# Performance work log

Hardware: AMD Instinct MI355X
Metric: run time of the kernel (lower is better)

The kernel has to match this reference:

```python
import jax, jax.numpy as jnp
import numpy as np

B, T, E, H, NT, NC = 256, 512, 200, 100, 100000, 5


def setup_inputs() -> dict:
    key = jax.random.key(0)
    ks = jax.random.split(key, 16)
    w = lambda i, shape: jax.random.normal(ks[i], shape, dtype=jnp.float32) * 0.05
    return {
        "txt": jax.random.randint(ks[0], (B, T), 0, NT),
        "lens": jax.random.randint(ks[1], (B,), 1, T + 1),
        "emb": w(2, (NT, E)),
        "W_ih": w(3, (3 * H, E)), "W_hh": w(4, (3 * H, H)),
        "b_ih": w(5, (3 * H,)), "b_hh": w(6, (3 * H,)),
        "W_lgr": w(7, (1, 2 * H)), "b_lgr": w(8, (1,)),
        "W_ts": w(9, (H, H)), "b_ts": w(10, (H,)),
        "W_ti": w(11, (H, H)), "b_ti": w(12, (H,)),
        "W_out": w(13, (NC, H)), "b_out": w(14, (NC,)),
    }


def reference(txt, lens, emb, W_ih, W_hh, b_ih, b_hh, W_lgr, b_lgr,
              W_ts, b_ts, W_ti, b_ti, W_out, b_out):
    bsz = txt.shape[0]
    # Embedding lookup with max_norm=1 renorm (torch nn.Embedding max_norm semantics)
    rows = emb[txt]  # (B,T,E)
    n = jnp.linalg.norm(rows, axis=-1, keepdims=True)
    emb_w = rows * jnp.where(n > 1.0, 1.0 / (n + 1e-7), 1.0)
    # eval mode: dropout is identity

    # ---- single-layer GRU (batch_first), gates in torch order r,z,n ----
    xp = emb_w @ W_ih.T + b_ih  # (B,T,3H), input projections precomputed

    def gru_step(h, x):
        hp = h @ W_hh.T + b_hh
        xr, xz, xn = jnp.split(x, 3, axis=-1)
        hr, hz, hn = jnp.split(hp, 3, axis=-1)
        r = jax.nn.sigmoid(xr + hr)
        z = jax.nn.sigmoid(xz + hz)
        ng = jnp.tanh(xn + r * hn)
        h = (1.0 - z) * ng + z * h
        return h, h

    h0 = jnp.zeros((bsz, H), jnp.float32)
    _, hs = jax.lax.scan(gru_step, h0, jnp.swapaxes(xp, 0, 1))
    rnn_out = jnp.swapaxes(hs, 0, 1)  # (B,T,H)

    # ---- cosine attention against an all-ones query ----
    inn = rnn_out / jnp.maximum(jnp.linalg.norm(rnn_out, axis=-1, keepdims=True), 1e-12)
    q = jnp.ones((bsz, H), jnp.float32)
    qn = q / jnp.maximum(jnp.linalg.norm(q, axis=-1, keepdims=True), 1e-12)
    att = jnp.einsum('bth,bh->bt', inn, qn) / H
    mask = (jnp.arange(T)[None, :] < lens[:, None]).astype(att.dtype)
    a_w = att * mask  # (B,T)

    # ---- gated-state recurrence ----
    z_all = jax.nn.relu(a_w)[..., None]          # (B,T,1)
    ti = rnn_out @ W_ti.T + b_ti                  # (B,T,H) trans_inp precomputed
    lgr_in = rnn_out @ W_lgr[:, :H].T             # (B,T,1) input half of lgr
    Wls = W_lgr[:, H:]                            # state half of lgr

    def rec_step(state, xs):
        ti_t, li_t, z_t = xs
        gate = jax.nn.sigmoid(li_t + state @ Wls.T + b_lgr)
        ns = jnp.tanh(ti_t + (gate * state) @ W_ts.T + b_ts)
        state = (1.0 - z_t) * state + z_t * ns
        return state, None

    xs = (jnp.swapaxes(ti, 0, 1), jnp.swapaxes(lgr_in, 0, 1), jnp.swapaxes(z_all, 0, 1))
    state, _ = jax.lax.scan(rec_step, jnp.zeros((bsz, H), jnp.float32), xs)
    return state @ W_out.T + b_out  # (B,NC)
```

## Files before the change

### kernel.cpp

```cpp
#include <hip/hip_runtime.h>

#define B_   256
#define T_   512
#define E_   200
#define H_   100
#define H3_  300
#define NC_  5

__device__ __forceinline__ void fma4(float4& acc, float a, const float4& w) {
    acc.x = fmaf(a, w.x, acc.x);
    acc.y = fmaf(a, w.y, acc.y);
    acc.z = fmaf(a, w.z, acc.z);
    acc.w = fmaf(a, w.w, acc.w);
}

#define KEEP4(v) asm volatile("" : "+v"((v).x), "+v"((v).y), "+v"((v).z), "+v"((v).w))

__device__ __forceinline__ void ldsbar() {
    asm volatile("s_waitcnt lgkmcnt(0)" ::: "memory");
    __builtin_amdgcn_s_barrier();
    __builtin_amdgcn_sched_barrier(0);
}

__global__ void k_pack(const float* __restrict__ W_ih, const float* __restrict__ W_ti,
                       const float* __restrict__ W_lgr,
                       float* __restrict__ wT, float* __restrict__ wcat) {
    int idx = blockIdx.x * 256 + threadIdx.x;
    if (idx < E_ * H3_) {
        int k = idx / H3_, j = idx - k * H3_;
        wT[idx] = W_ih[j * E_ + k];
    }
    int i2 = idx - E_ * H3_;
    if (i2 >= 0 && i2 < H_ * 104) {
        int k = i2 / 104, j = i2 - k * 104;
        float v = 0.0f;
        if (j < H_) v = W_ti[j * H_ + k];
        else if (j == H_) v = W_lgr[k];
        wcat[i2] = v;
    }
}

__global__ __launch_bounds__(320) void k_embgemm(
        const int* __restrict__ txt, const float* __restrict__ emb,
        const float* __restrict__ wT, const float* __restrict__ b_ih,
        float* __restrict__ xp) {
    __shared__ __align__(16) float A_lds[E_ * 36];
    __shared__ __align__(16) float W_lds[32 * 320];
    __shared__ float scale_lds[32];

    int tid = threadIdx.x;
    int base = blockIdx.x * 32;

    for (int idx = tid; idx < 32 * E_; idx += 320) {
        int r = idx / E_, k = idx - r * E_;
        int row = txt[base + r];
        A_lds[k * 36 + r] = emb[(size_t)row * E_ + k];
    }
    __syncthreads();

    if (tid < 32) {
        float ss = 0.0f;
        for (int k = 0; k < E_; ++k) { float v = A_lds[k * 36 + tid]; ss = fmaf(v, v, ss); }
        float n = sqrtf(ss);
        scale_lds[tid] = (n > 1.0f) ? (1.0f / (n + 1e-7f)) : 1.0f;
    }

    int c = tid % 80, g = tid / 80;
    float4 acc[8];
#pragma unroll
    for (int i = 0; i < 8; ++i) acc[i] = make_float4(0.f, 0.f, 0.f, 0.f);

    for (int kc = 0; kc < E_; kc += 32) {
        int KC = min(32, E_ - kc);
        __syncthreads();
        for (int idx = tid; idx < KC * H3_; idx += 320) {
            int kk = idx / H3_, j = idx - kk * H3_;
            W_lds[kk * 320 + j] = wT[(kc + kk) * H3_ + j];
        }
        __syncthreads();
        if (c < 75) {
            for (int kk = 0; kk < KC; ++kk) {
                int k = kc + kk;
                float4 wv = *(const float4*)&W_lds[kk * 320 + c * 4];
                float4 a0 = *(const float4*)&A_lds[k * 36 + g * 8];
                float4 a1 = *(const float4*)&A_lds[k * 36 + g * 8 + 4];
                fma4(acc[0], a0.x, wv); fma4(acc[1], a0.y, wv);
                fma4(acc[2], a0.z, wv); fma4(acc[3], a0.w, wv);
                fma4(acc[4], a1.x, wv); fma4(acc[5], a1.y, wv);
                fma4(acc[6], a1.z, wv); fma4(acc[7], a1.w, wv);
            }
        }
    }

    if (c < 75) {
        float4 bv = *(const float4*)&b_ih[c * 4];
#pragma unroll
        for (int rr = 0; rr < 8; ++rr) {
            int r = g * 8 + rr;
            float s = scale_lds[r];
            float4 res;
            res.x = fmaf(acc[rr].x, s, bv.x);
            res.y = fmaf(acc[rr].y, s, bv.y);
            res.z = fmaf(acc[rr].z, s, bv.z);
            res.w = fmaf(acc[rr].w, s, bv.w);
            *(float4*)&xp[(size_t)(base + r) * H3_ + c * 4] = res;
        }
    }
}

__global__ __launch_bounds__(640, 3)
void k_gru(
        const float* __restrict__ xp, const float* __restrict__ W_hh,
        const float* __restrict__ b_hh, float* __restrict__ rnn) {
    __shared__ __align__(16) float h_lds[104];
    __shared__ float p_lds[640];

    int tid = threadIdx.x;
    int half = (tid >= 320) ? 1 : 0;
    int j = tid - half * 320;
    int kb = half ? 48 : 0;
    int b = blockIdx.x;

    float4 w[13];
    if (j < H3_) {
        const float4* wr = (const float4*)(W_hh + (size_t)j * H_ + kb);
#pragma unroll
        for (int i = 0; i < 13; ++i) w[i] = wr[i];
        if (half) w[0] = make_float4(0.f, 0.f, 0.f, 0.f);
#pragma unroll
        for (int i = 0; i < 13; ++i) KEEP4(w[i]);
    } else {
#pragma unroll
        for (int i = 0; i < 13; ++i) w[i] = make_float4(0.f, 0.f, 0.f, 0.f);
    }

    float bhr = 0.f, bhz = 0.f, bhn = 0.f;
    if (tid < H_) { bhr = b_hh[tid]; bhz = b_hh[H_ + tid]; bhn = b_hh[2 * H_ + tid]; }

    if (tid < 104) h_lds[tid] = 0.0f;
    float hown = 0.0f;

    const float* xpb = xp + (size_t)b * T_ * H3_;
    float* rnnb = rnn + (size_t)b * T_ * H_;
    float xr = 0.f, xz = 0.f, xn = 0.f;
    if (tid < H_) { xr = xpb[tid]; xz = xpb[H_ + tid]; xn = xpb[2 * H_ + tid]; }
    __syncthreads();

    for (int t = 0; t < T_; ++t) {
        float a0 = 0.f, a1 = 0.f, a2 = 0.f, a3 = 0.f;
#pragma unroll
        for (int i = 0; i < 13; ++i) {
            float4 hv = *(const float4*)&h_lds[kb + i * 4];
            a0 = fmaf(w[i].x, hv.x, a0);
            a1 = fmaf(w[i].y, hv.y, a1);
            a2 = fmaf(w[i].z, hv.z, a2);
            a3 = fmaf(w[i].w, hv.w, a3);
        }
        float ownp = (a0 + a1) + (a2 + a3);
        if (j < H3_) p_lds[tid] = ownp;
        float nxr = 0.f, nxz = 0.f, nxn = 0.f;
        if (tid < H_ && t + 1 < T_) {
            const float* xq = xpb + (size_t)(t + 1) * H3_;
            nxr = xq[tid]; nxz = xq[H_ + tid]; nxn = xq[2 * H_ + tid];
        }
        ldsbar();
        if (tid < H_) {
            float hr = ownp             + p_lds[320 + tid] + bhr;
            float hz = p_lds[100 + tid] + p_lds[420 + tid] + bhz;
            float hn = p_lds[200 + tid] + p_lds[520 + tid] + bhn;
            float r = 1.0f / (1.0f + expf(-(xr + hr)));
            float z = 1.0f / (1.0f + expf(-(xz + hz)));
            float ng = tanhf(xn + r * hn);
            float hnew = (1.0f - z) * ng + z * hown;
            hown = hnew;
            h_lds[tid] = hnew;
            rnnb[(size_t)t * H_ + tid] = hnew;
            xr = nxr; xz = nxz; xn = nxn;
        }
        ldsbar();
    }
}

__global__ __launch_bounds__(256) void k_post(
        const float* __restrict__ rnn, const float* __restrict__ wcat,
        const float* __restrict__ b_ti, const int* __restrict__ lens,
        float* __restrict__ ti, float* __restrict__ lgr, float* __restrict__ zr) {
    __shared__ __align__(16) float A_lds[H_ * 72];
    __shared__ __align__(16) float W_lds[H_ * 112];

    int tid = threadIdx.x;
    int base = blockIdx.x * 64;

    for (int idx = tid; idx < 64 * H_; idx += 256) {
        int r = idx / H_, k = idx - r * H_;
        A_lds[k * 72 + r] = rnn[(size_t)(base + r) * H_ + k];
    }
    for (int idx = tid; idx < H_ * 104; idx += 256) {
        int k = idx / 104, jj = idx - k * 104;
        W_lds[k * 112 + jj] = wcat[idx];
    }
    __syncthreads();

    if (tid < 64) {
        float ss = 0.f, sm = 0.f;
        for (int k = 0; k < H_; ++k) {
            float v = A_lds[k * 72 + tid];
            ss = fmaf(v, v, ss); sm += v;
        }
        int row = base + tid;
        int bb = row >> 9, tt = row & 511;
        float att = sm / (fmaxf(sqrtf(ss), 1e-12f) * 1000.0f);
        zr[row] = (tt < lens[bb]) ? fmaxf(att, 0.0f) : 0.0f;
    }

    int c = tid % 32, g = tid / 32;
    float4 acc[8];
#pragma unroll
    for (int i = 0; i < 8; ++i) acc[i] = make_float4(0.f, 0.f, 0.f, 0.f);

    if (c < 26) {
        for (int k = 0; k < H_; ++k) {
            float4 wv = *(const float4*)&W_lds[k * 112 + c * 4];
            float4 a0 = *(const float4*)&A_lds[k * 72 + g * 8];
            float4 a1 = *(const float4*)&A_lds[k * 72 + g * 8 + 4];
            fma4(acc[0], a0.x, wv); fma4(acc[1], a0.y, wv);
            fma4(acc[2], a0.z, wv); fma4(acc[3], a0.w, wv);
            fma4(acc[4], a1.x, wv); fma4(acc[5], a1.y, wv);
            fma4(acc[6], a1.z, wv); fma4(acc[7], a1.w, wv);
        }
    }

    if (c < 25) {
        float4 bv = *(const float4*)&b_ti[c * 4];
#pragma unroll
        for (int rr = 0; rr < 8; ++rr) {
            int row = base + g * 8 + rr;
            float4 res;
            res.x = acc[rr].x + bv.x; res.y = acc[rr].y + bv.y;
            res.z = acc[rr].z + bv.z; res.w = acc[rr].w + bv.w;
            *(float4*)&ti[(size_t)row * H_ + c * 4] = res;
        }
    } else if (c == 25) {
#pragma unroll
        for (int rr = 0; rr < 8; ++rr) {
            int row = base + g * 8 + rr;
            lgr[row] = acc[rr].x;
        }
    }
}

__global__ __launch_bounds__(256, 1)
void k_rec(
        const float* __restrict__ ti, const float* __restrict__ lgr,
        const float* __restrict__ zr,
        const float* __restrict__ W_ts, const float* __restrict__ b_ts,
        const float* __restrict__ W_lgr, const float* __restrict__ b_lgr,
        const float* __restrict__ W_out, const float* __restrict__ b_out,
        float* __restrict__ out) {
    __shared__ __align__(16) float sA[104];
    __shared__ __align__(16) float sB[104];
    __shared__ float p_lds[256];
    __shared__ float red[2][2];

    int tid = threadIdx.x;
    int half = (tid >= 128) ? 1 : 0;
    int j = tid - half * 128;
    int kb = half ? 48 : 0;
    int b = blockIdx.x;

    float4 w[13];
    if (j < H_) {
        const float4* wr = (const float4*)(W_ts + (size_t)j * H_ + kb);
#pragma unroll
        for (int i = 0; i < 13; ++i) w[i] = wr[i];
        if (half) w[0] = make_float4(0.f, 0.f, 0.f, 0.f);
#pragma unroll
        for (int i = 0; i < 13; ++i) KEEP4(w[i]);
    } else {
#pragma unroll
        for (int i = 0; i < 13; ++i) w[i] = make_float4(0.f, 0.f, 0.f, 0.f);
    }

    float bts = 0.f, wlj = 0.f;
    if (tid < H_) { bts = b_ts[tid]; wlj = W_lgr[H_ + tid]; }
    float blg = b_lgr[0];
    if (tid < 104) sA[tid] = 0.0f;
    if (tid < 4) ((float*)red)[tid] = 0.0f;
    float sown = 0.0f;

    size_t rb = (size_t)b * T_;
    float tiv = 0.f, zt = 0.f, lt = 0.f;
    if (tid < H_) tiv = ti[rb * H_ + tid];
    zt = zr[rb]; lt = lgr[rb];
    __syncthreads();

    float* rd = sA;
    float* wrb = sB;
    for (int t = 0; t < T_; ++t) {
        float a0 = 0.f, a1 = 0.f, a2 = 0.f, a3 = 0.f;
#pragma unroll
        for (int i = 0; i < 13; ++i) {
            float4 s4 = *(const float4*)&rd[kb + i * 4];
            a0 = fmaf(w[i].x, s4.x, a0); a1 = fmaf(w[i].y, s4.y, a1);
            a2 = fmaf(w[i].z, s4.z, a2); a3 = fmaf(w[i].w, s4.w, a3);
        }
        float ownp = (a0 + a1) + (a2 + a3);
        if (half && j < H_) p_lds[tid] = ownp;
        float ntiv = 0.f, nzt = 0.f, nlt = 0.f;
        if (t + 1 < T_) {
            if (tid < H_) ntiv = ti[(rb + t + 1) * H_ + tid];
            nzt = zr[rb + t + 1]; nlt = lgr[rb + t + 1];
        }
        ldsbar();
        float dot = red[t & 1][0] + red[t & 1][1];
        float part = 0.0f;
        if (tid < H_) {
            float sv = ownp + p_lds[128 + tid];
            float gate = 1.0f / (1.0f + expf(-(lt + dot + blg)));
            float ns = tanhf(tiv + gate * sv + bts);
            float snew = (1.0f - zt) * sown + zt * ns;
            sown = snew;
            wrb[tid] = snew;
            part = wlj * snew;
        }
        tiv = ntiv; zt = nzt; lt = nlt;
#pragma unroll
        for (int off = 1; off < 64; off <<= 1) part += __shfl_xor(part, off, 64);
        if ((tid & 63) == 0 && tid < 128) red[(t + 1) & 1][tid >> 6] = part;
        ldsbar();
        float* tmp = rd; rd = wrb; wrb = tmp;
    }

    if (tid < NC_) {
        float o = b_out[tid];
        for (int k = 0; k < H_; ++k) o = fmaf(rd[k], W_out[tid * H_ + k], o);
        out[b * NC_ + tid] = o;
    }
}

extern "C" void kernel_launch(void* const* d_in, const int* in_sizes, int n_in,
                              void* d_out, int out_size, void* d_ws, size_t ws_size,
                              hipStream_t stream) {
    const int*   txt   = (const int*)d_in[0];
    const int*   lens  = (const int*)d_in[1];
    const float* emb   = (const float*)d_in[2];
    const float* W_ih  = (const float*)d_in[3];
    const float* W_hh  = (const float*)d_in[4];
    const float* b_ih  = (const float*)d_in[5];
    const float* b_hh  = (const float*)d_in[6];
    const float* W_lgr = (const float*)d_in[7];
    const float* b_lgr = (const float*)d_in[8];
    const float* W_ts  = (const float*)d_in[9];
    const float* b_ts  = (const float*)d_in[10];
    const float* W_ti  = (const float*)d_in[11];
    const float* b_ti  = (const float*)d_in[12];
    const float* W_out = (const float*)d_in[13];
    const float* b_out = (const float*)d_in[14];

    float* ws   = (float*)d_ws;
    float* xp   = ws;
    float* rnn  = xp + 39321600;
    float* lgrv = rnn + 13107200;
    float* zrv  = lgrv + 131072;
    float* wT   = zrv + 131072;
    float* wcat = wT + 60000;
    float* ti   = xp;

    float* out = (float*)d_out;

    k_pack<<<276, 256, 0, stream>>>(W_ih, W_ti, W_lgr, wT, wcat);
    k_embgemm<<<4096, 320, 0, stream>>>(txt, emb, wT, b_ih, xp);
    k_gru<<<256, 640, 0, stream>>>(xp, W_hh, b_hh, rnn);
    k_post<<<2048, 256, 0, stream>>>(rnn, wcat, b_ti, lens, ti, lgrv, zrv);
    k_rec<<<256, 256, 0, stream>>>(ti, lgrv, zrv, W_ts, b_ts, W_lgr, b_lgr,
                                   W_out, b_out, out);
}
```

Measured before the change: 1.682 ms.

## Double-buffer weight tiles with register prefetch in embedding GEMM kernel

```diff
diff --git a/kernel.cpp b/kernel.cpp
--- a/kernel.cpp
+++ b/kernel.cpp
@@ -6,6 +6,8 @@
 #define H_   100
 #define H3_  300
 #define NC_  5
+
+#define WSTRIDE 304
 
 __device__ __forceinline__ void fma4(float4& acc, float a, const float4& w) {
     acc.x = fmaf(a, w.x, acc.x);
@@ -45,22 +47,50 @@
         const float* __restrict__ wT, const float* __restrict__ b_ih,
         float* __restrict__ xp) {
     __shared__ __align__(16) float A_lds[E_ * 36];
-    __shared__ __align__(16) float W_lds[32 * 320];
+    __shared__ __align__(16) float W_lds[2][16 * WSTRIDE];
+    __shared__ float pp_lds[10][32];
     __shared__ float scale_lds[32];
 
     int tid = threadIdx.x;
     int base = blockIdx.x * 32;
 
-    for (int idx = tid; idx < 32 * E_; idx += 320) {
-        int r = idx / E_, k = idx - r * E_;
+#pragma unroll
+    for (int L = 0; L < 5; ++L) {
+        int q = tid + 320 * L;
+        int r = q / 50, k4 = q % 50;
         int row = txt[base + r];
-        A_lds[k * 36 + r] = emb[(size_t)row * E_ + k];
+        float4 v = ((const float4*)(emb + (size_t)row * E_))[k4];
+        int k = k4 * 4;
+        A_lds[(k + 0) * 36 + r] = v.x;
+        A_lds[(k + 1) * 36 + r] = v.y;
+        A_lds[(k + 2) * 36 + r] = v.z;
+        A_lds[(k + 3) * 36 + r] = v.w;
+    }
+#pragma unroll
+    for (int L = 0; L < 4; ++L) {
+        int f = tid + 320 * L;
+        if (f < 16 * 75) {
+            int kl = f / 75, j4 = f % 75;
+            float4 v = ((const float4*)wT)[kl * 75 + j4];
+            *(float4*)&W_lds[0][kl * WSTRIDE + j4 * 4] = v;
+        }
     }
     __syncthreads();
 
+    {
+        int r = tid % 32, s = tid / 32;
+        float ss = 0.f;
+        for (int k = s * 20; k < s * 20 + 20; ++k) {
+            float v = A_lds[k * 36 + r];
+            ss = fmaf(v, v, ss);
+        }
+        pp_lds[s][r] = ss;
+    }
+    __syncthreads();
     if (tid < 32) {
-        float ss = 0.0f;
-        for (int k = 0; k < E_; ++k) { float v = A_lds[k * 36 + tid]; ss = fmaf(v, v, ss); }
+        float ss = 0.f;
+#pragma unroll
+        for (int s = 0; s < 10; ++s) ss += pp_lds[s][tid];
         float n = sqrtf(ss);
         scale_lds[tid] = (n > 1.0f) ? (1.0f / (n + 1e-7f)) : 1.0f;
     }
@@ -70,18 +100,30 @@
 #pragma unroll
     for (int i = 0; i < 8; ++i) acc[i] = make_float4(0.f, 0.f, 0.f, 0.f);
 
-    for (int kc = 0; kc < E_; kc += 32) {
-        int KC = min(32, E_ - kc);
-        __syncthreads();
-        for (int idx = tid; idx < KC * H3_; idx += 320) {
-            int kk = idx / H3_, j = idx - kk * H3_;
-            W_lds[kk * 320 + j] = wT[(kc + kk) * H3_ + j];
-        }
-        __syncthreads();
+    const int NT = 13;
+    for (int ic = 0; ic < NT; ++ic) {
+        int KC = (ic == 12) ? 8 : 16;
+        int cur = ic & 1;
+
+        float4 pf0, pf1, pf2, pf3;
+        int nKC = 0;
+        if (ic + 1 < NT) {
+            nKC = (ic + 1 == 12) ? 8 : 16;
+            const float4* src = ((const float4*)wT) + (ic + 1) * 16 * 75;
+            int f0 = tid;
+            if (f0 < nKC * 75) pf0 = src[f0];
+            int f1 = tid + 320;
+            if (f1 < nKC * 75) pf1 = src[f1];
+            int f2 = tid + 640;
+            if (f2 < nKC * 75) pf2 = src[f2];
+            int f3 = tid + 960;
+            if (f3 < nKC * 75) pf3 = src[f3];
+        }
+
         if (c < 75) {
             for (int kk = 0; kk < KC; ++kk) {
-                int k = kc + kk;
-                float4 wv = *(const float4*)&W_lds[kk * 320 + c * 4];
+                int k = ic * 16 + kk;
+                float4 wv = *(const float4*)&W_lds[cur][kk * WSTRIDE + c * 4];
                 float4 a0 = *(const float4*)&A_lds[k * 36 + g * 8];
                 float4 a1 = *(const float4*)&A_lds[k * 36 + g * 8 + 4];
                 fma4(acc[0], a0.x, wv); fma4(acc[1], a0.y, wv);
@@ -90,6 +132,18 @@
                 fma4(acc[6], a1.z, wv); fma4(acc[7], a1.w, wv);
             }
         }
+
+        if (ic + 1 < NT) {
+            int f0 = tid;
+            if (f0 < nKC * 75) *(float4*)&W_lds[cur ^ 1][(f0 / 75) * WSTRIDE + (f0 % 75) * 4] = pf0;
+            int f1 = tid + 320;
+            if (f1 < nKC * 75) *(float4*)&W_lds[cur ^ 1][(f1 / 75) * WSTRIDE + (f1 % 75) * 4] = pf1;
+            int f2 = tid + 640;
+            if (f2 < nKC * 75) *(float4*)&W_lds[cur ^ 1][(f2 / 75) * WSTRIDE + (f2 % 75) * 4] = pf2;
+            int f3 = tid + 960;
+            if (f3 < nKC * 75) *(float4*)&W_lds[cur ^ 1][(f3 / 75) * WSTRIDE + (f3 % 75) * 4] = pf3;
+        }
+        ldsbar();
     }
 
     if (c < 75) {
```

Measured after the change: 1.528 ms. -9.1%, faster.
